# Kernel optimization log

Measured on AMD Instinct MI355X. Metric: run time of the kernel, lower is better.

The kernel has to match this reference:

```python
import jax, jax.numpy as jnp
import numpy as np

LN_EPS = 1e-5


def setup_inputs() -> dict:
    key = jax.random.key(0)
    ks = jax.random.split(key, 6)
    n_nodes, mem_dim = 500000, 256
    n_upd, msg_dim = 65536, 512
    return {
        "unique_node_ids": jnp.arange(n_upd, dtype=jnp.int64) if jax.config.jax_enable_x64 else jnp.arange(n_upd, dtype=jnp.int32),
        "unique_messages": jax.random.normal(ks[0], (n_upd, msg_dim), dtype=jnp.float32),
        "timestamps": jax.random.uniform(ks[1], (n_upd,), dtype=jnp.float32),
        "memory": jax.random.normal(ks[2], (n_nodes, mem_dim), dtype=jnp.float32),
        "last_update": jnp.zeros((n_nodes,), dtype=jnp.float32),
        "W_ih": jax.random.normal(ks[3], (3 * mem_dim, msg_dim), dtype=jnp.float32) * (1.0 / np.sqrt(msg_dim)),
        "W_hh": jax.random.normal(ks[4], (3 * mem_dim, mem_dim), dtype=jnp.float32) * (1.0 / np.sqrt(mem_dim)),
        "b_ih": jnp.zeros((3 * mem_dim,), dtype=jnp.float32),
        "b_hh": jnp.zeros((3 * mem_dim,), dtype=jnp.float32),
        "ln_gamma": jnp.ones((mem_dim,), dtype=jnp.float32),
        "ln_beta": jnp.zeros((mem_dim,), dtype=jnp.float32),
    }


def _gru_cell(x, h, W_ih, W_hh, b_ih, b_hh):
    # torch.nn.GRUCell math
    gi = x @ W_ih.T + b_ih          # [N, 3H]
    gh = h @ W_hh.T + b_hh          # [N, 3H]
    i_r, i_z, i_n = jnp.split(gi, 3, axis=-1)
    h_r, h_z, h_n = jnp.split(gh, 3, axis=-1)
    r = jax.nn.sigmoid(i_r + h_r)
    z = jax.nn.sigmoid(i_z + h_z)
    n = jnp.tanh(i_n + r * h_n)
    return (1.0 - z) * n + z * h


def _layer_norm(x, gamma, beta):
    mu = jnp.mean(x, axis=-1, keepdims=True)
    var = jnp.mean(jnp.square(x - mu), axis=-1, keepdims=True)
    return (x - mu) * jax.lax.rsqrt(var + LN_EPS) * gamma + beta


def reference(unique_node_ids, unique_messages, timestamps, memory, last_update,
              W_ih, W_hh, b_ih, b_hh, ln_gamma, ln_beta):
    # gather memory rows for the nodes being updated
    h = memory[unique_node_ids]                      # [N, H]
    new_h = _gru_cell(unique_messages, h, W_ih, W_hh, b_ih, b_hh)
    new_h = _layer_norm(new_h, ln_gamma, ln_beta)
    # scatter updated rows back (get_updated_memory semantics: pure copy)
    updated_memory = memory.at[unique_node_ids].set(new_h)
    updated_last_update = last_update.at[unique_node_ids].set(timestamps)
    return updated_memory, updated_last_update
```

## Files before the change

### kernel.cpp

```cpp
#include <hip/hip_runtime.h>
#include <hip/hip_bf16.h>

typedef float  f32x4 __attribute__((ext_vector_type(4)));
typedef short  s16x8 __attribute__((ext_vector_type(8)));

#define MEMH   256
#define MSGD   512
#define G3     768
#define W_IH_ELEMS (G3*MSGD)
#define W_HH_ELEMS (G3*MEMH)
#define W_TOT_ELEMS (W_IH_ELEMS + W_HH_ELEMS)
#define W_BYTES    ((size_t)W_TOT_ELEMS * 2)

#define BM     64
#define NTHR   1024
#define AH_OFF 0
#define AM_OFF 32768
#define O_OFF  32768
#define LDS_BYTES (32768 + 66560)

static __device__ __forceinline__ short f2bf(float x) {
    __hip_bfloat16 b = __float2bfloat16(x);
    return __builtin_bit_cast(short, b);
}
static __device__ __forceinline__ float bf2f(short s) {
    unsigned int u = ((unsigned int)(unsigned short)s) << 16;
    return __builtin_bit_cast(float, u);
}
static __device__ __forceinline__ float sigf(float x) {
    return 1.f / (1.f + __expf(-x));
}
static __device__ __forceinline__ float tanh_fast(float x) {
    float e = __expf(-2.f * fabsf(x));
    float t = (1.f - e) / (1.f + e);
    return copysignf(t, x);
}
static __device__ __forceinline__ f32x4 ntload4(const float* p) {
    return __builtin_nontemporal_load((const f32x4*)p);
}
static __device__ __forceinline__ void ntstore4(float* p, f32x4 v) {
    __builtin_nontemporal_store(v, (f32x4*)p);
}

__global__ void smu_copy_kernel(const float* __restrict__ mem,
                                const float* __restrict__ lu,
                                float* __restrict__ out_mem,
                                float* __restrict__ out_lu,
                                long n_mem4, long n_lu4) {
    long i = (long)blockIdx.x * blockDim.x + threadIdx.x;
    long stride = (long)gridDim.x * blockDim.x;
    long total = n_mem4 + n_lu4;
    for (; i < total; i += stride) {
        if (i < n_mem4) ntstore4(out_mem + i * 4, ntload4(mem + i * 4));
        else {
            long j = (i - n_mem4) * 4;
            ntstore4(out_lu + j, ntload4(lu + j));
        }
    }
}

__global__ __launch_bounds__(256)
void smu_copy_skip_kernel(const float* __restrict__ mem,
                          const float* __restrict__ lu,
                          const unsigned* __restrict__ bm,
                          float* __restrict__ out_mem,
                          float* __restrict__ out_lu,
                          long n_nodes) {
    const long nu = n_nodes * (MEMH / 4);
    const long stride = (long)gridDim.x * blockDim.x;
    const long i0 = (long)blockIdx.x * blockDim.x + threadIdx.x;

    for (long i = i0; i < nu; i += stride * 4) {
        long  u0 = i, u1 = i + stride, u2 = i + stride * 2, u3 = i + stride * 3;
        f32x4 v0, v1, v2, v3;
        bool  f0 = false, f1 = false, f2 = false, f3 = false;
        {
            long r = u0 >> 6;
            f0 = !((bm[r >> 5] >> (r & 31)) & 1u);
            if (f0) v0 = ntload4(mem + u0 * 4);
        }
        if (u1 < nu) {
            long r = u1 >> 6;
            f1 = !((bm[r >> 5] >> (r & 31)) & 1u);
            if (f1) v1 = ntload4(mem + u1 * 4);
        }
        if (u2 < nu) {
            long r = u2 >> 6;
            f2 = !((bm[r >> 5] >> (r & 31)) & 1u);
            if (f2) v2 = ntload4(mem + u2 * 4);
        }
        if (u3 < nu) {
            long r = u3 >> 6;
            f3 = !((bm[r >> 5] >> (r & 31)) & 1u);
            if (f3) v3 = ntload4(mem + u3 * 4);
        }
        if (f0) ntstore4(out_mem + u0 * 4, v0);
        if (f1) ntstore4(out_mem + u1 * 4, v1);
        if (f2) ntstore4(out_mem + u2 * 4, v2);
        if (f3) ntstore4(out_mem + u3 * 4, v3);
    }
    for (long i = i0; i < n_nodes; i += stride) {
        if (!((bm[i >> 5] >> (i & 31)) & 1u)) {
            float v = __builtin_nontemporal_load(lu + i);
            __builtin_nontemporal_store(v, out_lu + i);
        }
    }
}

__global__ void smu_cvtw_kernel(const float* __restrict__ wih,
                                const float* __restrict__ whh,
                                short* __restrict__ o) {
    int i = blockIdx.x * blockDim.x + threadIdx.x;
    if (i >= W_TOT_ELEMS) return;
    if (i < W_IH_ELEMS) {
        int f = i >> 9, r = i & 511, l = r >> 3, e = r & 7;
        int t = f >> 4, k = f & 15;
        int row = t * 16 + (l & 15), col = k * 32 + (l >> 4) * 8 + e;
        o[i] = f2bf(wih[row * MSGD + col]);
    } else {
        int j = i - W_IH_ELEMS;
        int f = j >> 9, r = j & 511, l = r >> 3, e = r & 7;
        int t = f >> 3, k = f & 7;
        int row = t * 16 + (l & 15), col = k * 32 + (l >> 4) * 8 + e;
        o[i] = f2bf(whh[row * MEMH + col]);
    }
}

__global__ void smu_bits_kernel(const int* __restrict__ ids,
                                unsigned* __restrict__ bm, int n) {
    int i = blockIdx.x * blockDim.x + threadIdx.x;
    if (i < n) {
        int id = ids[i];
        atomicOr(&bm[id >> 5], 1u << (id & 31));
    }
}

template<bool USE_WS>
static __device__ __forceinline__ s16x8 load_b(const float* __restrict__ Wf,
                                               const short* __restrict__ Wb,
                                               int t, int k, int ldk, int nkt, int lane) {
    if constexpr (USE_WS) {
        return *(const s16x8*)(Wb + ((size_t)(t * nkt + k) << 9) + lane * 8);
    } else {
        int row = t * 16 + (lane & 15);
        int col = k * 32 + (lane >> 4) * 8;
        f32x4 x = *(const f32x4*)(Wf + (size_t)row * ldk + col);
        f32x4 y = *(const f32x4*)(Wf + (size_t)row * ldk + col + 4);
        s16x8 s;
        s[0]=f2bf(x[0]); s[1]=f2bf(x[1]); s[2]=f2bf(x[2]); s[3]=f2bf(x[3]);
        s[4]=f2bf(y[0]); s[5]=f2bf(y[1]); s[6]=f2bf(y[2]); s[7]=f2bf(y[3]);
        return s;
    }
}

template<bool USE_WS>
__global__ __launch_bounds__(NTHR, 1)
void smu_gru_kernel(const int*   __restrict__ ids,
                    const float* __restrict__ msg,
                    const float* __restrict__ ts,
                    const float* __restrict__ memory,
                    const float* __restrict__ W_ih,
                    const float* __restrict__ W_hh,
                    const float* __restrict__ b_ih,
                    const float* __restrict__ b_hh,
                    const float* __restrict__ gamma,
                    const float* __restrict__ beta,
                    const short* __restrict__ wsw,
                    float* __restrict__ out_mem,
                    float* __restrict__ out_lu) {
    __shared__ __align__(16) unsigned char lds[LDS_BYTES];
    const int tid  = threadIdx.x;
    const int bid  = blockIdx.x;
    const long base = (long)bid * BM;

    {
        const float* src = msg + base * MSGD;
        #pragma unroll
        for (int it = 0; it < 4; ++it) {
            int u = tid + NTHR * it;
            int row = u >> 6;
            f32x4 a = ntload4(src + u * 8);
            f32x4 b = ntload4(src + u * 8 + 4);
            s16x8 s;
            s[0]=f2bf(a[0]); s[1]=f2bf(a[1]); s[2]=f2bf(a[2]); s[3]=f2bf(a[3]);
            s[4]=f2bf(b[0]); s[5]=f2bf(b[1]); s[6]=f2bf(b[2]); s[7]=f2bf(b[3]);
            int byte = AM_OFF + ((u * 16) ^ ((row & 7) << 4));
            *(s16x8*)(lds + byte) = s;
        }
        #pragma unroll
        for (int it = 0; it < 2; ++it) {
            int u = tid + NTHR * it;
            int row = u >> 5;
            int c8  = u & 31;
            int id  = ids[base + row];
            const float* hs = memory + (size_t)id * MEMH + c8 * 8;
            f32x4 a = ntload4(hs);
            f32x4 b = ntload4(hs + 4);
            s16x8 s;
            s[0]=f2bf(a[0]); s[1]=f2bf(a[1]); s[2]=f2bf(a[2]); s[3]=f2bf(a[3]);
            s[4]=f2bf(b[0]); s[5]=f2bf(b[1]); s[6]=f2bf(b[2]); s[7]=f2bf(b[3]);
            int byte = AH_OFF + ((u * 16) ^ ((row & 7) << 4));
            *(s16x8*)(lds + byte) = s;
        }
    }
    __syncthreads();

    const int lane = tid & 63;
    const int w    = tid >> 6;
    const int lr   = lane & 15;
    const int lk8  = (lane >> 4) * 8;
    const int sw   = (lr & 7) << 4;
    const short* Wi = wsw;
    const short* Wh = wsw + W_IH_ELEMS;

    f32x4 acc[4][3] = {};
    f32x4 accn[4]   = {};

    {
        s16x8 b[2][3];
        #pragma unroll
        for (int i = 0; i < 3; ++i) b[0][i] = load_b<USE_WS>(W_ih, Wi, w + 16*i, 0, MSGD, 16, lane);
        #pragma unroll
        for (int i = 0; i < 3; ++i) b[1][i] = load_b<USE_WS>(W_ih, Wi, w + 16*i, 1, MSGD, 16, lane);
        #pragma unroll
        for (int k = 0; k < 16; ++k) {
            const int cb = (k * 32 + lk8) * 2;
            #pragma unroll
            for (int m = 0; m < 4; ++m) {
                s16x8 a = *(const s16x8*)(lds + AM_OFF + (((m*16 + lr) * 1024 + cb) ^ sw));
                #pragma unroll
                for (int i = 0; i < 3; ++i)
                    acc[m][i] = __builtin_amdgcn_mfma_f32_16x16x32_bf16(a, b[k & 1][i], acc[m][i], 0, 0, 0);
            }
            if (k < 14) {
                #pragma unroll
                for (int i = 0; i < 3; ++i)
                    b[k & 1][i] = load_b<USE_WS>(W_ih, Wi, w + 16*i, k + 2, MSGD, 16, lane);
            }
        }
    }
    {
        s16x8 b[2][3];
        #pragma unroll
        for (int i = 0; i < 3; ++i) b[0][i] = load_b<USE_WS>(W_hh, Wh, w + 16*i, 0, MEMH, 8, lane);
        #pragma unroll
        for (int i = 0; i < 3; ++i) b[1][i] = load_b<USE_WS>(W_hh, Wh, w + 16*i, 1, MEMH, 8, lane);
        #pragma unroll
        for (int k = 0; k < 8; ++k) {
            const int cb = (k * 32 + lk8) * 2;
            #pragma unroll
            for (int m = 0; m < 4; ++m) {
                s16x8 a = *(const s16x8*)(lds + AH_OFF + (((m*16 + lr) * 512 + cb) ^ sw));
                acc[m][0] = __builtin_amdgcn_mfma_f32_16x16x32_bf16(a, b[k & 1][0], acc[m][0], 0, 0, 0);
                acc[m][1] = __builtin_amdgcn_mfma_f32_16x16x32_bf16(a, b[k & 1][1], acc[m][1], 0, 0, 0);
                accn[m]   = __builtin_amdgcn_mfma_f32_16x16x32_bf16(a, b[k & 1][2], accn[m],   0, 0, 0);
            }
            if (k < 6) {
                #pragma unroll
                for (int i = 0; i < 3; ++i)
                    b[k & 1][i] = load_b<USE_WS>(W_hh, Wh, w + 16*i, k + 2, MEMH, 8, lane);
            }
        }
    }

    __syncthreads();

    {
        const int lq = (lane >> 4) * 4;
        const int j  = w * 16 + lr;
        const float br = b_ih[j]       + b_hh[j];
        const float bz = b_ih[256 + j] + b_hh[256 + j];
        const float bihn = b_ih[512 + j], bhhn = b_hh[512 + j];
        #pragma unroll
        for (int m = 0; m < 4; ++m) {
            #pragma unroll
            for (int q = 0; q < 4; ++q) {
                int row = m * 16 + lq + q;
                float r = sigf(acc[m][0][q] + br);
                float z = sigf(acc[m][1][q] + bz);
                float n = tanh_fast(acc[m][2][q] + bihn + r * (accn[m][q] + bhhn));
                float hv = bf2f(*(const short*)(lds + AH_OFF + ((row * 512 + j * 2) ^ ((row & 7) << 4))));
                float o = (1.f - z) * n + z * hv;
                *(float*)(lds + O_OFF + (row * 260 + j) * 4) = o;
            }
        }
    }
    __syncthreads();

    #pragma unroll
    for (int rr = 0; rr < 4; ++rr) {
        int row = w * 4 + rr;
        f32x4 x = *(const f32x4*)(lds + O_OFF + (row * 260 + lane * 4) * 4);
        float s1 = x[0] + x[1] + x[2] + x[3];
        float s2 = x[0]*x[0] + x[1]*x[1] + x[2]*x[2] + x[3]*x[3];
        #pragma unroll
        for (int mm = 32; mm > 0; mm >>= 1) {
            s1 += __shfl_xor(s1, mm);
            s2 += __shfl_xor(s2, mm);
        }
        float mu  = s1 * (1.f / 256.f);
        float var = fmaxf(s2 * (1.f / 256.f) - mu * mu, 0.f);
        float inv = rsqrtf(var + 1e-5f);
        f32x4 g  = *(const f32x4*)(gamma + lane * 4);
        f32x4 be = *(const f32x4*)(beta  + lane * 4);
        int id = ids[base + row];
        f32x4 y;
        #pragma unroll
        for (int c = 0; c < 4; ++c) y[c] = (x[c] - mu) * inv * g[c] + be[c];
        ntstore4(out_mem + (size_t)id * MEMH + lane * 4, y);
        if (lane == 0) __builtin_nontemporal_store(ts[base + row], out_lu + id);
    }
}

extern "C" void kernel_launch(void* const* d_in, const int* in_sizes, int n_in,
                              void* d_out, int out_size, void* d_ws, size_t ws_size,
                              hipStream_t stream) {
    (void)n_in; (void)out_size;
    const int*   ids = (const int*)  d_in[0];
    const float* msg = (const float*)d_in[1];
    const float* ts  = (const float*)d_in[2];
    const float* mem = (const float*)d_in[3];
    const float* lu  = (const float*)d_in[4];
    const float* Wih = (const float*)d_in[5];
    const float* Whh = (const float*)d_in[6];
    const float* bih = (const float*)d_in[7];
    const float* bhh = (const float*)d_in[8];
    const float* gam = (const float*)d_in[9];
    const float* bet = (const float*)d_in[10];

    const int  n_upd   = in_sizes[0];
    const long n_nodes = (long)in_sizes[3] / MEMH;

    float* out_mem = (float*)d_out;
    float* out_lu  = out_mem + (size_t)n_nodes * MEMH;

    const size_t bm_words = (size_t)((n_nodes + 31) / 32);
    const size_t bm_bytes_pad = bm_words * 4 + 16;
    const bool ws_w  = (d_ws != nullptr) && (ws_size >= W_BYTES);
    const bool ws_bm = (d_ws != nullptr) && (ws_size >= W_BYTES + bm_bytes_pad);

    short*    wsw = (short*)d_ws;
    unsigned* bm  = (unsigned*)((char*)d_ws + W_BYTES);

    const int grid = n_upd / BM;

    if (ws_w) {
        smu_cvtw_kernel<<<(W_TOT_ELEMS + 255) / 256, 256, 0, stream>>>(Wih, Whh, wsw);
    }

    if (ws_bm) {
        (void)hipMemsetAsync(bm, 0, bm_bytes_pad, stream);
        smu_bits_kernel<<<(n_upd + 255) / 256, 256, 0, stream>>>(ids, bm, n_upd);
        smu_gru_kernel<true><<<grid, NTHR, 0, stream>>>(
            ids, msg, ts, mem, Wih, Whh, bih, bhh, gam, bet, wsw, out_mem, out_lu);
        smu_copy_skip_kernel<<<2048, 256, 0, stream>>>(mem, lu, bm, out_mem, out_lu, n_nodes);
    } else {
        long n_mem4 = n_nodes * (MEMH / 4);
        long n_lu4  = n_nodes / 4;
        smu_copy_kernel<<<2048, 256, 0, stream>>>(mem, lu, out_mem, out_lu, n_mem4, n_lu4);
        if (ws_w) {
            smu_gru_kernel<true><<<grid, NTHR, 0, stream>>>(
                ids, msg, ts, mem, Wih, Whh, bih, bhh, gam, bet, wsw, out_mem, out_lu);
        } else {
            smu_gru_kernel<false><<<grid, NTHR, 0, stream>>>(
                ids, msg, ts, mem, Wih, Whh, bih, bhh, gam, bet, nullptr, out_mem, out_lu);
        }
    }
}
```

Before: 350.8 us.

## Fuse GRU compute and skip-copy into one kernel with interleaved block roles

Merges the GRU/LayerNorm kernel and the bitmap-filtered memory copy into a single launch: odd blocks copy the untouched memory rows and timestamps, even blocks run the MFMA GRU tile. The aim is to overlap the bandwidth-bound copy with the compute-bound GEMM and drop a kernel launch boundary. It also swaps hipMemsetAsync for a small clear kernel. The copy blocks now run at 1024 threads with the same LDS allocation, which may reduce copy occupancy, and the two roles compete for CUs.

```diff
diff --git a/kernel.cpp b/kernel.cpp
--- a/kernel.cpp
+++ b/kernel.cpp
@@ -55,54 +55,6 @@
         else {
             long j = (i - n_mem4) * 4;
             ntstore4(out_lu + j, ntload4(lu + j));
-        }
-    }
-}
-
-__global__ __launch_bounds__(256)
-void smu_copy_skip_kernel(const float* __restrict__ mem,
-                          const float* __restrict__ lu,
-                          const unsigned* __restrict__ bm,
-                          float* __restrict__ out_mem,
-                          float* __restrict__ out_lu,
-                          long n_nodes) {
-    const long nu = n_nodes * (MEMH / 4);
-    const long stride = (long)gridDim.x * blockDim.x;
-    const long i0 = (long)blockIdx.x * blockDim.x + threadIdx.x;
-
-    for (long i = i0; i < nu; i += stride * 4) {
-        long  u0 = i, u1 = i + stride, u2 = i + stride * 2, u3 = i + stride * 3;
-        f32x4 v0, v1, v2, v3;
-        bool  f0 = false, f1 = false, f2 = false, f3 = false;
-        {
-            long r = u0 >> 6;
-            f0 = !((bm[r >> 5] >> (r & 31)) & 1u);
-            if (f0) v0 = ntload4(mem + u0 * 4);
-        }
-        if (u1 < nu) {
-            long r = u1 >> 6;
-            f1 = !((bm[r >> 5] >> (r & 31)) & 1u);
-            if (f1) v1 = ntload4(mem + u1 * 4);
-        }
-        if (u2 < nu) {
-            long r = u2 >> 6;
-            f2 = !((bm[r >> 5] >> (r & 31)) & 1u);
-            if (f2) v2 = ntload4(mem + u2 * 4);
-        }
-        if (u3 < nu) {
-            long r = u3 >> 6;
-            f3 = !((bm[r >> 5] >> (r & 31)) & 1u);
-            if (f3) v3 = ntload4(mem + u3 * 4);
-        }
-        if (f0) ntstore4(out_mem + u0 * 4, v0);
-        if (f1) ntstore4(out_mem + u1 * 4, v1);
-        if (f2) ntstore4(out_mem + u2 * 4, v2);
-        if (f3) ntstore4(out_mem + u3 * 4, v3);
-    }
-    for (long i = i0; i < n_nodes; i += stride) {
-        if (!((bm[i >> 5] >> (i & 31)) & 1u)) {
-            float v = __builtin_nontemporal_load(lu + i);
-            __builtin_nontemporal_store(v, out_lu + i);
         }
     }
 }
@@ -126,6 +78,10 @@
     }
 }
 
+__global__ void smu_clear_kernel(unsigned* __restrict__ p, int n) {
+    int i = blockIdx.x * blockDim.x + threadIdx.x;
+    if (i < n) p[i] = 0u;
+}
 __global__ void smu_bits_kernel(const int* __restrict__ ids,
                                 unsigned* __restrict__ bm, int n) {
     int i = blockIdx.x * blockDim.x + threadIdx.x;
@@ -150,6 +106,214 @@
         s[0]=f2bf(x[0]); s[1]=f2bf(x[1]); s[2]=f2bf(x[2]); s[3]=f2bf(x[3]);
         s[4]=f2bf(y[0]); s[5]=f2bf(y[1]); s[6]=f2bf(y[2]); s[7]=f2bf(y[3]);
         return s;
+    }
+}
+
+template<bool USE_WS>
+__global__ __launch_bounds__(NTHR, 1)
+void smu_fused_kernel(const int*   __restrict__ ids,
+                      const float* __restrict__ msg,
+                      const float* __restrict__ ts,
+                      const float* __restrict__ memory,
+                      const float* __restrict__ lu,
+                      const float* __restrict__ W_ih,
+                      const float* __restrict__ W_hh,
+                      const float* __restrict__ b_ih,
+                      const float* __restrict__ b_hh,
+                      const float* __restrict__ gamma,
+                      const float* __restrict__ beta,
+                      const short* __restrict__ wsw,
+                      const unsigned* __restrict__ bm,
+                      float* __restrict__ out_mem,
+                      float* __restrict__ out_lu,
+                      long n_nodes) {
+    __shared__ __align__(16) unsigned char lds[LDS_BYTES];
+    const int tid = threadIdx.x;
+    const int bid = blockIdx.x;
+
+    if (bid & 1) {
+        const long nblk   = gridDim.x >> 1;
+        const long cid    = bid >> 1;
+        const long nu     = n_nodes * (MEMH / 4);
+        const long stride = nblk * NTHR;
+        const long i0     = cid * NTHR + tid;
+
+        for (long i = i0; i < nu; i += stride * 4) {
+            long  u0 = i, u1 = i + stride, u2 = i + stride * 2, u3 = i + stride * 3;
+            f32x4 v0, v1, v2, v3;
+            bool  f0 = false, f1 = false, f2 = false, f3 = false;
+            {
+                long r = u0 >> 6;
+                f0 = !((bm[r >> 5] >> (r & 31)) & 1u);
+                if (f0) v0 = ntload4(memory + u0 * 4);
+            }
+            if (u1 < nu) {
+                long r = u1 >> 6;
+                f1 = !((bm[r >> 5] >> (r & 31)) & 1u);
+                if (f1) v1 = ntload4(memory + u1 * 4);
+            }
+            if (u2 < nu) {
+                long r = u2 >> 6;
+                f2 = !((bm[r >> 5] >> (r & 31)) & 1u);
+                if (f2) v2 = ntload4(memory + u2 * 4);
+            }
+            if (u3 < nu) {
+                long r = u3 >> 6;
+                f3 = !((bm[r >> 5] >> (r & 31)) & 1u);
+                if (f3) v3 = ntload4(memory + u3 * 4);
+            }
+            if (f0) ntstore4(out_mem + u0 * 4, v0);
+            if (f1) ntstore4(out_mem + u1 * 4, v1);
+            if (f2) ntstore4(out_mem + u2 * 4, v2);
+            if (f3) ntstore4(out_mem + u3 * 4, v3);
+        }
+        for (long i = i0; i < n_nodes; i += stride) {
+            if (!((bm[i >> 5] >> (i & 31)) & 1u)) {
+                float v = __builtin_nontemporal_load(lu + i);
+                __builtin_nontemporal_store(v, out_lu + i);
+            }
+        }
+        return;
+    }
+
+    const long base = (long)(bid >> 1) * BM;
+
+    {
+        const float* src = msg + base * MSGD;
+        #pragma unroll
+        for (int it = 0; it < 4; ++it) {
+            int u = tid + NTHR * it;
+            int row = u >> 6;
+            f32x4 a = ntload4(src + u * 8);
+            f32x4 b = ntload4(src + u * 8 + 4);
+            s16x8 s;
+            s[0]=f2bf(a[0]); s[1]=f2bf(a[1]); s[2]=f2bf(a[2]); s[3]=f2bf(a[3]);
+            s[4]=f2bf(b[0]); s[5]=f2bf(b[1]); s[6]=f2bf(b[2]); s[7]=f2bf(b[3]);
+            int byte = AM_OFF + ((u * 16) ^ ((row & 7) << 4));
+            *(s16x8*)(lds + byte) = s;
+        }
+        #pragma unroll
+        for (int it = 0; it < 2; ++it) {
+            int u = tid + NTHR * it;
+            int row = u >> 5;
+            int c8  = u & 31;
+            int id  = ids[base + row];
+            const float* hs = memory + (size_t)id * MEMH + c8 * 8;
+            f32x4 a = ntload4(hs);
+            f32x4 b = ntload4(hs + 4);
+            s16x8 s;
+            s[0]=f2bf(a[0]); s[1]=f2bf(a[1]); s[2]=f2bf(a[2]); s[3]=f2bf(a[3]);
+            s[4]=f2bf(b[0]); s[5]=f2bf(b[1]); s[6]=f2bf(b[2]); s[7]=f2bf(b[3]);
+            int byte = AH_OFF + ((u * 16) ^ ((row & 7) << 4));
+            *(s16x8*)(lds + byte) = s;
+        }
+    }
+    __syncthreads();
+
+    const int lane = tid & 63;
+    const int w    = tid >> 6;
+    const int lr   = lane & 15;
+    const int lk8  = (lane >> 4) * 8;
+    const int sw   = (lr & 7) << 4;
+    const short* Wi = wsw;
+    const short* Wh = wsw + W_IH_ELEMS;
+
+    f32x4 acc[4][3] = {};
+    f32x4 accn[4]   = {};
+
+    {
+        s16x8 b[2][3];
+        #pragma unroll
+        for (int i = 0; i < 3; ++i) b[0][i] = load_b<USE_WS>(W_ih, Wi, w + 16*i, 0, MSGD, 16, lane);
+        #pragma unroll
+        for (int i = 0; i < 3; ++i) b[1][i] = load_b<USE_WS>(W_ih, Wi, w + 16*i, 1, MSGD, 16, lane);
+        #pragma unroll
+        for (int k = 0; k < 16; ++k) {
+            const int cb = (k * 32 + lk8) * 2;
+            #pragma unroll
+            for (int m = 0; m < 4; ++m) {
+                s16x8 a = *(const s16x8*)(lds + AM_OFF + (((m*16 + lr) * 1024 + cb) ^ sw));
+                #pragma unroll
+                for (int i = 0; i < 3; ++i)
+                    acc[m][i] = __builtin_amdgcn_mfma_f32_16x16x32_bf16(a, b[k & 1][i], acc[m][i], 0, 0, 0);
+            }
+            if (k < 14) {
+                #pragma unroll
+                for (int i = 0; i < 3; ++i)
+                    b[k & 1][i] = load_b<USE_WS>(W_ih, Wi, w + 16*i, k + 2, MSGD, 16, lane);
+            }
+        }
+    }
+    {
+        s16x8 b[2][3];
+        #pragma unroll
+        for (int i = 0; i < 3; ++i) b[0][i] = load_b<USE_WS>(W_hh, Wh, w + 16*i, 0, MEMH, 8, lane);
+        #pragma unroll
+        for (int i = 0; i < 3; ++i) b[1][i] = load_b<USE_WS>(W_hh, Wh, w + 16*i, 1, MEMH, 8, lane);
+        #pragma unroll
+        for (int k = 0; k < 8; ++k) {
+            const int cb = (k * 32 + lk8) * 2;
+            #pragma unroll
+            for (int m = 0; m < 4; ++m) {
+                s16x8 a = *(const s16x8*)(lds + AH_OFF + (((m*16 + lr) * 512 + cb) ^ sw));
+                acc[m][0] = __builtin_amdgcn_mfma_f32_16x16x32_bf16(a, b[k & 1][0], acc[m][0], 0, 0, 0);
+                acc[m][1] = __builtin_amdgcn_mfma_f32_16x16x32_bf16(a, b[k & 1][1], acc[m][1], 0, 0, 0);
+                accn[m]   = __builtin_amdgcn_mfma_f32_16x16x32_bf16(a, b[k & 1][2], accn[m],   0, 0, 0);
+            }
+            if (k < 6) {
+                #pragma unroll
+                for (int i = 0; i < 3; ++i)
+                    b[k & 1][i] = load_b<USE_WS>(W_hh, Wh, w + 16*i, k + 2, MEMH, 8, lane);
+            }
+        }
+    }
+
+    __syncthreads();
+
+    {
+        const int lq = (lane >> 4) * 4;
+        const int j  = w * 16 + lr;
+        const float br = b_ih[j]       + b_hh[j];
+        const float bz = b_ih[256 + j] + b_hh[256 + j];
+        const float bihn = b_ih[512 + j], bhhn = b_hh[512 + j];
+        #pragma unroll
+        for (int m = 0; m < 4; ++m) {
+            #pragma unroll
+            for (int q = 0; q < 4; ++q) {
+                int row = m * 16 + lq + q;
+                float r = sigf(acc[m][0][q] + br);
+                float z = sigf(acc[m][1][q] + bz);
+                float n = tanh_fast(acc[m][2][q] + bihn + r * (accn[m][q] + bhhn));
+                float hv = bf2f(*(const short*)(lds + AH_OFF + ((row * 512 + j * 2) ^ ((row & 7) << 4))));
+                float o = (1.f - z) * n + z * hv;
+                *(float*)(lds + O_OFF + (row * 260 + j) * 4) = o;
+            }
+        }
+    }
+    __syncthreads();
+
+    #pragma unroll
+    for (int rr = 0; rr < 4; ++rr) {
+        int row = w * 4 + rr;
+        f32x4 x = *(const f32x4*)(lds + O_OFF + (row * 260 + lane * 4) * 4);
+        float s1 = x[0] + x[1] + x[2] + x[3];
+        float s2 = x[0]*x[0] + x[1]*x[1] + x[2]*x[2] + x[3]*x[3];
+        #pragma unroll
+        for (int mm = 32; mm > 0; mm >>= 1) {
+            s1 += __shfl_xor(s1, mm);
+            s2 += __shfl_xor(s2, mm);
+        }
+        float mu  = s1 * (1.f / 256.f);
+        float var = fmaxf(s2 * (1.f / 256.f) - mu * mu, 0.f);
+        float inv = rsqrtf(var + 1e-5f);
+        f32x4 g  = *(const f32x4*)(gamma + lane * 4);
+        f32x4 be = *(const f32x4*)(beta  + lane * 4);
+        int id = ids[base + row];
+        f32x4 y;
+        #pragma unroll
+        for (int c = 0; c < 4; ++c) y[c] = (x[c] - mu) * inv * g[c] + be[c];
+        ntstore4(out_mem + (size_t)id * MEMH + lane * 4, y);
+        if (lane == 0) __builtin_nontemporal_store(ts[base + row], out_lu + id);
     }
 }
 
@@ -169,9 +333,8 @@
                     float* __restrict__ out_mem,
                     float* __restrict__ out_lu) {
     __shared__ __align__(16) unsigned char lds[LDS_BYTES];
-    const int tid  = threadIdx.x;
-    const int bid  = blockIdx.x;
-    const long base = (long)bid * BM;
+    const int tid = threadIdx.x;
+    const long base = (long)blockIdx.x * BM;
 
     {
         const float* src = msg + base * MSGD;
@@ -334,8 +497,8 @@
     float* out_mem = (float*)d_out;
     float* out_lu  = out_mem + (size_t)n_nodes * MEMH;
 
-    const size_t bm_words = (size_t)((n_nodes + 31) / 32);
-    const size_t bm_bytes_pad = bm_words * 4 + 16;
+    const int    bm_words     = (int)((n_nodes + 31) / 32) + 4;
+    const size_t bm_bytes_pad = (size_t)bm_words * 4;
     const bool ws_w  = (d_ws != nullptr) && (ws_size >= W_BYTES);
     const bool ws_bm = (d_ws != nullptr) && (ws_size >= W_BYTES + bm_bytes_pad);
 
@@ -349,11 +512,11 @@
     }
 
     if (ws_bm) {
-        (void)hipMemsetAsync(bm, 0, bm_bytes_pad, stream);
+        smu_clear_kernel<<<(bm_words + 255) / 256, 256, 0, stream>>>(bm, bm_words);
         smu_bits_kernel<<<(n_upd + 255) / 256, 256, 0, stream>>>(ids, bm, n_upd);
-        smu_gru_kernel<true><<<grid, NTHR, 0, stream>>>(
-            ids, msg, ts, mem, Wih, Whh, bih, bhh, gam, bet, wsw, out_mem, out_lu);
-        smu_copy_skip_kernel<<<2048, 256, 0, stream>>>(mem, lu, bm, out_mem, out_lu, n_nodes);
+        smu_fused_kernel<true><<<2 * grid, NTHR, 0, stream>>>(
+            ids, msg, ts, mem, lu, Wih, Whh, bih, bhh, gam, bet,
+            wsw, bm, out_mem, out_lu, n_nodes);
     } else {
         long n_mem4 = n_nodes * (MEMH / 4);
         long n_lu4  = n_nodes / 4;
```

Result: faster. 326.8 us (-6.8%).

## Fuse skip-copy into GRU kernel with interleaved blocks and smaller tiles

Applied to the files above, without the earlier changes.

Merges the bitmap-guarded memory copy and the GRU/LayerNorm compute into one launch. Block indices are interleaved so copy blocks and compute blocks run at the same time, letting bandwidth-bound copying overlap MFMA work. The GRU tile drops from 64 rows with 1024 threads to 32 rows with 512 threads, keeping results in registers. LayerNorm becomes a cross-wave partial-sum reduction through LDS instead of staging the full output tile, and the memset is replaced by a clear kernel. The trade-off is scalar scattered stores and more per-block reduction overhead.

```diff
diff --git a/kernel.cpp b/kernel.cpp
--- a/kernel.cpp
+++ b/kernel.cpp
@@ -12,12 +12,13 @@
 #define W_TOT_ELEMS (W_IH_ELEMS + W_HH_ELEMS)
 #define W_BYTES    ((size_t)W_TOT_ELEMS * 2)
 
-#define BM     64
-#define NTHR   1024
-#define AH_OFF 0
-#define AM_OFF 32768
-#define O_OFF  32768
-#define LDS_BYTES (32768 + 66560)
+#define BM     32
+#define NTHR   512
+#define AM_OFF 0
+#define AH_OFF 32768
+#define PART_OFF 49152
+#define STAT_OFF 51200
+#define LDS_BYTES 51456
 
 static __device__ __forceinline__ short f2bf(float x) {
     __hip_bfloat16 b = __float2bfloat16(x);
@@ -55,54 +56,6 @@
         else {
             long j = (i - n_mem4) * 4;
             ntstore4(out_lu + j, ntload4(lu + j));
-        }
-    }
-}
-
-__global__ __launch_bounds__(256)
-void smu_copy_skip_kernel(const float* __restrict__ mem,
-                          const float* __restrict__ lu,
-                          const unsigned* __restrict__ bm,
-                          float* __restrict__ out_mem,
-                          float* __restrict__ out_lu,
-                          long n_nodes) {
-    const long nu = n_nodes * (MEMH / 4);
-    const long stride = (long)gridDim.x * blockDim.x;
-    const long i0 = (long)blockIdx.x * blockDim.x + threadIdx.x;
-
-    for (long i = i0; i < nu; i += stride * 4) {
-        long  u0 = i, u1 = i + stride, u2 = i + stride * 2, u3 = i + stride * 3;
-        f32x4 v0, v1, v2, v3;
-        bool  f0 = false, f1 = false, f2 = false, f3 = false;
-        {
-            long r = u0 >> 6;
-            f0 = !((bm[r >> 5] >> (r & 31)) & 1u);
-            if (f0) v0 = ntload4(mem + u0 * 4);
-        }
-        if (u1 < nu) {
-            long r = u1 >> 6;
-            f1 = !((bm[r >> 5] >> (r & 31)) & 1u);
-            if (f1) v1 = ntload4(mem + u1 * 4);
-        }
-        if (u2 < nu) {
-            long r = u2 >> 6;
-            f2 = !((bm[r >> 5] >> (r & 31)) & 1u);
-            if (f2) v2 = ntload4(mem + u2 * 4);
-        }
-        if (u3 < nu) {
-            long r = u3 >> 6;
-            f3 = !((bm[r >> 5] >> (r & 31)) & 1u);
-            if (f3) v3 = ntload4(mem + u3 * 4);
-        }
-        if (f0) ntstore4(out_mem + u0 * 4, v0);
-        if (f1) ntstore4(out_mem + u1 * 4, v1);
-        if (f2) ntstore4(out_mem + u2 * 4, v2);
-        if (f3) ntstore4(out_mem + u3 * 4, v3);
-    }
-    for (long i = i0; i < n_nodes; i += stride) {
-        if (!((bm[i >> 5] >> (i & 31)) & 1u)) {
-            float v = __builtin_nontemporal_load(lu + i);
-            __builtin_nontemporal_store(v, out_lu + i);
         }
     }
 }
@@ -126,6 +79,10 @@
     }
 }
 
+__global__ void smu_clear_kernel(unsigned* __restrict__ p, int n) {
+    int i = blockIdx.x * blockDim.x + threadIdx.x;
+    if (i < n) p[i] = 0u;
+}
 __global__ void smu_bits_kernel(const int* __restrict__ ids,
                                 unsigned* __restrict__ bm, int n) {
     int i = blockIdx.x * blockDim.x + threadIdx.x;
@@ -153,25 +110,80 @@
     }
 }
 
-template<bool USE_WS>
-__global__ __launch_bounds__(NTHR, 1)
-void smu_gru_kernel(const int*   __restrict__ ids,
-                    const float* __restrict__ msg,
-                    const float* __restrict__ ts,
-                    const float* __restrict__ memory,
-                    const float* __restrict__ W_ih,
-                    const float* __restrict__ W_hh,
-                    const float* __restrict__ b_ih,
-                    const float* __restrict__ b_hh,
-                    const float* __restrict__ gamma,
-                    const float* __restrict__ beta,
-                    const short* __restrict__ wsw,
-                    float* __restrict__ out_mem,
-                    float* __restrict__ out_lu) {
+template<bool USE_WS, bool SPLIT>
+__global__ __launch_bounds__(NTHR, 4)
+void smu_fused_kernel(const int*   __restrict__ ids,
+                      const float* __restrict__ msg,
+                      const float* __restrict__ ts,
+                      const float* __restrict__ memory,
+                      const float* __restrict__ lu,
+                      const float* __restrict__ W_ih,
+                      const float* __restrict__ W_hh,
+                      const float* __restrict__ b_ih,
+                      const float* __restrict__ b_hh,
+                      const float* __restrict__ gamma,
+                      const float* __restrict__ beta,
+                      const short* __restrict__ wsw,
+                      const unsigned* __restrict__ bm,
+                      float* __restrict__ out_mem,
+                      float* __restrict__ out_lu,
+                      long n_nodes, int n_copy_blk) {
     __shared__ __align__(16) unsigned char lds[LDS_BYTES];
-    const int tid  = threadIdx.x;
-    const int bid  = blockIdx.x;
-    const long base = (long)bid * BM;
+    const int tid = threadIdx.x;
+    const int bid = blockIdx.x;
+
+    int local;
+    if constexpr (SPLIT) {
+        const int s = bid >> 9;
+        const int r = bid & 511;
+        local = s * 256 + (r & 255);
+        if (r >= 256) {
+            const long nu     = n_nodes * (MEMH / 4);
+            const long stride = (long)n_copy_blk * NTHR;
+            const long i0     = (long)local * NTHR + tid;
+
+            for (long i = i0; i < nu; i += stride * 4) {
+                long  u0 = i, u1 = i + stride, u2 = i + stride * 2, u3 = i + stride * 3;
+                f32x4 v0, v1, v2, v3;
+                bool  f0 = false, f1 = false, f2 = false, f3 = false;
+                {
+                    long r0 = u0 >> 6;
+                    f0 = !((bm[r0 >> 5] >> (r0 & 31)) & 1u);
+                    if (f0) v0 = ntload4(memory + u0 * 4);
+                }
+                if (u1 < nu) {
+                    long r1 = u1 >> 6;
+                    f1 = !((bm[r1 >> 5] >> (r1 & 31)) & 1u);
+                    if (f1) v1 = ntload4(memory + u1 * 4);
+                }
+                if (u2 < nu) {
+                    long r2 = u2 >> 6;
+                    f2 = !((bm[r2 >> 5] >> (r2 & 31)) & 1u);
+                    if (f2) v2 = ntload4(memory + u2 * 4);
+                }
+                if (u3 < nu) {
+                    long r3 = u3 >> 6;
+                    f3 = !((bm[r3 >> 5] >> (r3 & 31)) & 1u);
+                    if (f3) v3 = ntload4(memory + u3 * 4);
+                }
+                if (f0) ntstore4(out_mem + u0 * 4, v0);
+                if (f1) ntstore4(out_mem + u1 * 4, v1);
+                if (f2) ntstore4(out_mem + u2 * 4, v2);
+                if (f3) ntstore4(out_mem + u3 * 4, v3);
+            }
+            for (long i = i0; i < n_nodes; i += stride) {
+                if (!((bm[i >> 5] >> (i & 31)) & 1u)) {
+                    float v = __builtin_nontemporal_load(lu + i);
+                    __builtin_nontemporal_store(v, out_lu + i);
+                }
+            }
+            return;
+        }
+    } else {
+        local = bid;
+    }
+
+    const long base = (long)local * BM;
 
     {
         const float* src = msg + base * MSGD;
@@ -213,102 +225,155 @@
     const short* Wi = wsw;
     const short* Wh = wsw + W_IH_ELEMS;
 
-    f32x4 acc[4][3] = {};
-    f32x4 accn[4]   = {};
-
-    {
-        s16x8 b[2][3];
-        #pragma unroll
-        for (int i = 0; i < 3; ++i) b[0][i] = load_b<USE_WS>(W_ih, Wi, w + 16*i, 0, MSGD, 16, lane);
-        #pragma unroll
-        for (int i = 0; i < 3; ++i) b[1][i] = load_b<USE_WS>(W_ih, Wi, w + 16*i, 1, MSGD, 16, lane);
+    f32x4 rz[2][2][2] = {};
+    f32x4 gin[2][2]   = {};
+    f32x4 ghn[2][2]   = {};
+
+    {
+        s16x8 b[2][6];
+        #pragma unroll
+        for (int i = 0; i < 6; ++i)
+            b[0][i] = load_b<USE_WS>(W_ih, Wi, w + 8*(i/3) + 16*(i%3), 0, MSGD, 16, lane);
+        #pragma unroll
+        for (int i = 0; i < 6; ++i)
+            b[1][i] = load_b<USE_WS>(W_ih, Wi, w + 8*(i/3) + 16*(i%3), 1, MSGD, 16, lane);
         #pragma unroll
         for (int k = 0; k < 16; ++k) {
             const int cb = (k * 32 + lk8) * 2;
             #pragma unroll
-            for (int m = 0; m < 4; ++m) {
+            for (int m = 0; m < 2; ++m) {
                 s16x8 a = *(const s16x8*)(lds + AM_OFF + (((m*16 + lr) * 1024 + cb) ^ sw));
                 #pragma unroll
-                for (int i = 0; i < 3; ++i)
-                    acc[m][i] = __builtin_amdgcn_mfma_f32_16x16x32_bf16(a, b[k & 1][i], acc[m][i], 0, 0, 0);
+                for (int ci = 0; ci < 2; ++ci) {
+                    rz[m][ci][0] = __builtin_amdgcn_mfma_f32_16x16x32_bf16(a, b[k & 1][ci*3+0], rz[m][ci][0], 0, 0, 0);
+                    rz[m][ci][1] = __builtin_amdgcn_mfma_f32_16x16x32_bf16(a, b[k & 1][ci*3+1], rz[m][ci][1], 0, 0, 0);
+                    gin[m][ci]   = __builtin_amdgcn_mfma_f32_16x16x32_bf16(a, b[k & 1][ci*3+2], gin[m][ci],   0, 0, 0);
+                }
             }
             if (k < 14) {
                 #pragma unroll
-                for (int i = 0; i < 3; ++i)
-                    b[k & 1][i] = load_b<USE_WS>(W_ih, Wi, w + 16*i, k + 2, MSGD, 16, lane);
-            }
-        }
-    }
-    {
-        s16x8 b[2][3];
-        #pragma unroll
-        for (int i = 0; i < 3; ++i) b[0][i] = load_b<USE_WS>(W_hh, Wh, w + 16*i, 0, MEMH, 8, lane);
-        #pragma unroll
-        for (int i = 0; i < 3; ++i) b[1][i] = load_b<USE_WS>(W_hh, Wh, w + 16*i, 1, MEMH, 8, lane);
+                for (int i = 0; i < 6; ++i)
+                    b[k & 1][i] = load_b<USE_WS>(W_ih, Wi, w + 8*(i/3) + 16*(i%3), k + 2, MSGD, 16, lane);
+            }
+        }
+    }
+    {
+        s16x8 b[2][6];
+        #pragma unroll
+        for (int i = 0; i < 6; ++i)
+            b[0][i] = load_b<USE_WS>(W_hh, Wh, w + 8*(i/3) + 16*(i%3), 0, MEMH, 8, lane);
+        #pragma unroll
+        for (int i = 0; i < 6; ++i)
+            b[1][i] = load_b<USE_WS>(W_hh, Wh, w + 8*(i/3) + 16*(i%3), 1, MEMH, 8, lane);
         #pragma unroll
         for (int k = 0; k < 8; ++k) {
             const int cb = (k * 32 + lk8) * 2;
             #pragma unroll
-            for (int m = 0; m < 4; ++m) {
+            for (int m = 0; m < 2; ++m) {
                 s16x8 a = *(const s16x8*)(lds + AH_OFF + (((m*16 + lr) * 512 + cb) ^ sw));
-                acc[m][0] = __builtin_amdgcn_mfma_f32_16x16x32_bf16(a, b[k & 1][0], acc[m][0], 0, 0, 0);
-                acc[m][1] = __builtin_amdgcn_mfma_f32_16x16x32_bf16(a, b[k & 1][1], acc[m][1], 0, 0, 0);
-                accn[m]   = __builtin_amdgcn_mfma_f32_16x16x32_bf16(a, b[k & 1][2], accn[m],   0, 0, 0);
+                #pragma unroll
+                for (int ci = 0; ci < 2; ++ci) {
+                    rz[m][ci][0] = __builtin_amdgcn_mfma_f32_16x16x32_bf16(a, b[k & 1][ci*3+0], rz[m][ci][0], 0, 0, 0);
+                    rz[m][ci][1] = __builtin_amdgcn_mfma_f32_16x16x32_bf16(a, b[k & 1][ci*3+1], rz[m][ci][1], 0, 0, 0);
+                    ghn[m][ci]   = __builtin_amdgcn_mfma_f32_16x16x32_bf16(a, b[k & 1][ci*3+2], ghn[m][ci],   0, 0, 0);
+                }
             }
             if (k < 6) {
                 #pragma unroll
-                for (int i = 0; i < 3; ++i)
-                    b[k & 1][i] = load_b<USE_WS>(W_hh, Wh, w + 16*i, k + 2, MEMH, 8, lane);
-            }
-        }
-    }
-
-    __syncthreads();
-
-    {
-        const int lq = (lane >> 4) * 4;
-        const int j  = w * 16 + lr;
-        const float br = b_ih[j]       + b_hh[j];
-        const float bz = b_ih[256 + j] + b_hh[256 + j];
-        const float bihn = b_ih[512 + j], bhhn = b_hh[512 + j];
-        #pragma unroll
-        for (int m = 0; m < 4; ++m) {
+                for (int i = 0; i < 6; ++i)
+                    b[k & 1][i] = load_b<USE_WS>(W_hh, Wh, w + 8*(i/3) + 16*(i%3), k + 2, MEMH, 8, lane);
+            }
+        }
+    }
+
+    const int lq = (lane >> 4);
+    f32x4 o_[2][2];
+    {
+        #pragma unroll
+        for (int ci = 0; ci < 2; ++ci) {
+            const int j = (w + 8*ci) * 16 + lr;
+            const float br = b_ih[j]       + b_hh[j];
+            const float bz = b_ih[256 + j] + b_hh[256 + j];
+            const float bihn = b_ih[512 + j], bhhn = b_hh[512 + j];
+            #pragma unroll
+            for (int m = 0; m < 2; ++m) {
+                #pragma unroll
+                for (int q = 0; q < 4; ++q) {
+                    int row = m * 16 + lq * 4 + q;
+                    float r = sigf(rz[m][ci][0][q] + br);
+                    float z = sigf(rz[m][ci][1][q] + bz);
+                    float n = tanh_fast(gin[m][ci][q] + bihn + r * (ghn[m][ci][q] + bhhn));
+                    float hv = bf2f(*(const short*)(lds + AH_OFF + ((row * 512 + j * 2) ^ ((row & 7) << 4))));
+                    o_[m][ci][q] = (1.f - z) * n + z * hv;
+                }
+            }
+        }
+    }
+
+    {
+        float* part = (float*)(lds + PART_OFF);
+        #pragma unroll
+        for (int m = 0; m < 2; ++m) {
             #pragma unroll
             for (int q = 0; q < 4; ++q) {
-                int row = m * 16 + lq + q;
-                float r = sigf(acc[m][0][q] + br);
-                float z = sigf(acc[m][1][q] + bz);
-                float n = tanh_fast(acc[m][2][q] + bihn + r * (accn[m][q] + bhhn));
-                float hv = bf2f(*(const short*)(lds + AH_OFF + ((row * 512 + j * 2) ^ ((row & 7) << 4))));
-                float o = (1.f - z) * n + z * hv;
-                *(float*)(lds + O_OFF + (row * 260 + j) * 4) = o;
+                float v0 = o_[m][0][q], v1 = o_[m][1][q];
+                float s1 = v0 + v1;
+                float s2 = v0 * v0 + v1 * v1;
+                #pragma unroll
+                for (int mk = 1; mk < 16; mk <<= 1) {
+                    s1 += __shfl_xor(s1, mk);
+                    s2 += __shfl_xor(s2, mk);
+                }
+                if (lr == 0) {
+                    int row = m * 16 + lq * 4 + q;
+                    part[(row * 8 + w) * 2]     = s1;
+                    part[(row * 8 + w) * 2 + 1] = s2;
+                }
             }
         }
     }
     __syncthreads();
 
-    #pragma unroll
-    for (int rr = 0; rr < 4; ++rr) {
-        int row = w * 4 + rr;
-        f32x4 x = *(const f32x4*)(lds + O_OFF + (row * 260 + lane * 4) * 4);
-        float s1 = x[0] + x[1] + x[2] + x[3];
-        float s2 = x[0]*x[0] + x[1]*x[1] + x[2]*x[2] + x[3]*x[3];
-        #pragma unroll
-        for (int mm = 32; mm > 0; mm >>= 1) {
-            s1 += __shfl_xor(s1, mm);
-            s2 += __shfl_xor(s2, mm);
+    if (w == 0 && lane < 32) {
+        const float* part = (const float*)(lds + PART_OFF);
+        float s1 = 0.f, s2 = 0.f;
+        #pragma unroll
+        for (int i = 0; i < 8; ++i) {
+            s1 += part[(lane * 8 + i) * 2];
+            s2 += part[(lane * 8 + i) * 2 + 1];
         }
         float mu  = s1 * (1.f / 256.f);
         float var = fmaxf(s2 * (1.f / 256.f) - mu * mu, 0.f);
         float inv = rsqrtf(var + 1e-5f);
-        f32x4 g  = *(const f32x4*)(gamma + lane * 4);
-        f32x4 be = *(const f32x4*)(beta  + lane * 4);
-        int id = ids[base + row];
-        f32x4 y;
-        #pragma unroll
-        for (int c = 0; c < 4; ++c) y[c] = (x[c] - mu) * inv * g[c] + be[c];
-        ntstore4(out_mem + (size_t)id * MEMH + lane * 4, y);
-        if (lane == 0) __builtin_nontemporal_store(ts[base + row], out_lu + id);
+        float* st = (float*)(lds + STAT_OFF);
+        st[lane * 2]     = mu;
+        st[lane * 2 + 1] = inv;
+    }
+    __syncthreads();
+
+    {
+        const float* st = (const float*)(lds + STAT_OFF);
+        #pragma unroll
+        for (int ci = 0; ci < 2; ++ci) {
+            const int j = (w + 8*ci) * 16 + lr;
+            const float ga = gamma[j], be = beta[j];
+            #pragma unroll
+            for (int m = 0; m < 2; ++m) {
+                #pragma unroll
+                for (int q = 0; q < 4; ++q) {
+                    int row = m * 16 + lq * 4 + q;
+                    float mu  = st[row * 2];
+                    float inv = st[row * 2 + 1];
+                    int id = ids[base + row];
+                    float y = (o_[m][ci][q] - mu) * inv * ga + be;
+                    __builtin_nontemporal_store(y, out_mem + (size_t)id * MEMH + j);
+                }
+            }
+        }
+        if (w == 0 && lane < 32) {
+            int id = ids[base + lane];
+            __builtin_nontemporal_store(ts[base + lane], out_lu + id);
+        }
     }
 }
 
@@ -334,36 +399,38 @@
     float* out_mem = (float*)d_out;
     float* out_lu  = out_mem + (size_t)n_nodes * MEMH;
 
-    const size_t bm_words = (size_t)((n_nodes + 31) / 32);
-    const size_t bm_bytes_pad = bm_words * 4 + 16;
+    const int    bm_words     = (int)((n_nodes + 31) / 32) + 4;
+    const size_t bm_bytes_pad = (size_t)bm_words * 4;
     const bool ws_w  = (d_ws != nullptr) && (ws_size >= W_BYTES);
     const bool ws_bm = (d_ws != nullptr) && (ws_size >= W_BYTES + bm_bytes_pad);
 
     short*    wsw = (short*)d_ws;
     unsigned* bm  = (unsigned*)((char*)d_ws + W_BYTES);
 
-    const int grid = n_upd / BM;
+    const int grid_gru = n_upd / BM;
 
     if (ws_w) {
         smu_cvtw_kernel<<<(W_TOT_ELEMS + 255) / 256, 256, 0, stream>>>(Wih, Whh, wsw);
     }
 
     if (ws_bm) {
-        (void)hipMemsetAsync(bm, 0, bm_bytes_pad, stream);
+        smu_clear_kernel<<<(bm_words + 255) / 256, 256, 0, stream>>>(bm, bm_words);
         smu_bits_kernel<<<(n_upd + 255) / 256, 256, 0, stream>>>(ids, bm, n_upd);
-        smu_gru_kernel<true><<<grid, NTHR, 0, stream>>>(
-            ids, msg, ts, mem, Wih, Whh, bih, bhh, gam, bet, wsw, out_mem, out_lu);
-        smu_copy_skip_kernel<<<2048, 256, 0, stream>>>(mem, lu, bm, out_mem, out_lu, n_nodes);
+        smu_fused_kernel<true, true><<<2 * grid_gru, NTHR, 0, stream>>>(
+            ids, msg, ts, mem, lu, Wih, Whh, bih, bhh, gam, bet,
+            wsw, bm, out_mem, out_lu, n_nodes, grid_gru);
     } else {
         long n_mem4 = n_nodes * (MEMH / 4);
         long n_lu4  = n_nodes / 4;
         smu_copy_kernel<<<2048, 256, 0, stream>>>(mem, lu, out_mem, out_lu, n_mem4, n_lu4);
         if (ws_w) {
-            smu_gru_kernel<true><<<grid, NTHR, 0, stream>>>(
-                ids, msg, ts, mem, Wih, Whh, bih, bhh, gam, bet, wsw, out_mem, out_lu);
+            smu_fused_kernel<true, false><<<grid_gru, NTHR, 0, stream>>>(
+                ids, msg, ts, mem, lu, Wih, Whh, bih, bhh, gam, bet,
+                wsw, nullptr, out_mem, out_lu, n_nodes, 0);
         } else {
-            smu_gru_kernel<false><<<grid, NTHR, 0, stream>>>(
-                ids, msg, ts, mem, Wih, Whh, bih, bhh, gam, bet, nullptr, out_mem, out_lu);
-        }
-    }
-}
+            smu_fused_kernel<false, false><<<grid_gru, NTHR, 0, stream>>>(
+                ids, msg, ts, mem, lu, Wih, Whh, bih, bhh, gam, bet,
+                nullptr, nullptr, out_mem, out_lu, n_nodes, 0);
+        }
+    }
+}
```

New measurement: 344.8 us. No clear change (-1.7%).
